# Performance work log

Measured on AMD Instinct MI355X. Metric: run time of the kernel, lower is better.

## Reference

```python
import jax, jax.numpy as jnp
import numpy as np

B, S, D, E, H, K = 4, 2048, 1024, 8, 1024, 2


def setup_inputs() -> dict:
    key = jax.random.key(0)
    k0, k1, k2, k3 = jax.random.split(key, 4)
    x = jax.random.normal(k0, (B, S, D), dtype=jnp.float32)
    router_w = jax.random.normal(k1, (E, D), dtype=jnp.float32) * 0.02
    w1 = jax.random.normal(k2, (D, E * H), dtype=jnp.float32) * 0.02
    w2 = jax.random.normal(k3, (E * H, D), dtype=jnp.float32) * 0.02
    expert_bias = jnp.zeros((E,), dtype=jnp.float32)
    return {"x": x, "router_w": router_w, "w1": w1, "w2": w2, "expert_bias": expert_bias}


def reference(x, router_w, w1, w2, expert_bias):
    b, s, d = x.shape
    e = router_w.shape[0]
    x_flat = x.reshape(-1, d)                      # [T, D]
    T = x_flat.shape[0]

    # Router: sigmoid scores, bias-balanced top-k selection
    router_logits = x_flat @ router_w.T            # [T, E]
    router_probs = jax.nn.sigmoid(router_logits.astype(jnp.float32))
    selection_scores = router_probs + expert_bias[None, :]
    _, selected = jax.lax.top_k(selection_scores, K)          # [T, K] indices
    top_k_w = jnp.take_along_axis(router_probs, selected, axis=-1)
    top_k_w = top_k_w / (top_k_w.sum(-1, keepdims=True) + 1e-20)
    top_k_w = top_k_w.astype(x.dtype)

    # Combine weights as a sparse [T, E] matrix (equivalent to the
    # padded_gather / grouped-GEMM / padded_scatter pipeline since
    # unselected experts get weight 0).
    combine = jnp.zeros((T, e), dtype=x.dtype).at[
        jnp.arange(T)[:, None], selected].add(top_k_w)

    # Expert MLP: relu(x @ w1)^2 @ w2, experts are contiguous column blocks
    h = jnp.square(jax.nn.relu(x_flat @ w1))       # [T, E*H]
    h = h.reshape(T, e, H) * combine[:, :, None]   # weighted per-expert hidden
    y = jnp.einsum('teh,ehd->td', h, w2.reshape(e, H, d))
    output = y.reshape(b, s, d)

    # Aux losses
    router_z_loss = jnp.mean(jnp.square(jax.nn.logsumexp(router_logits, axis=-1)))
    sel_flat = selected.reshape(-1)
    tokens_per_expert = jnp.zeros((e,), jnp.float32).at[sel_flat].add(1.0)
    f_i = (tokens_per_expert / tokens_per_expert.sum()).astype(x.dtype)

    # bias-balancing branch: per-sequence load balance loss
    sel_seq = selected.reshape(b, s * K)
    f_seq = jnp.zeros((b, e), jnp.float32).at[
        jnp.arange(b)[:, None], sel_seq].add(1.0) / (s * K)
    p_seq = router_probs.reshape(b, s, e).mean(axis=1)
    load_balance_loss = e * (f_seq * p_seq).sum(-1).mean()

    # uniform expert widths -> normalized widths are all 1
    widths_norm = jnp.ones((e,), jnp.float32)
    compute_loss = (router_probs @ widths_norm).mean()

    return output, router_z_loss, load_balance_loss, compute_loss, f_i
```

## Files before the change

kernel.cpp:

```cpp
#include <hip/hip_runtime.h>

typedef unsigned short u16;
typedef unsigned int u32;
typedef __bf16 bf16x8 __attribute__((ext_vector_type(8)));
typedef float f32x4 __attribute__((ext_vector_type(4)));

#define NTOK   8192
#define DDIM   1024
#define NEXP   8
#define HDIM   1024
#define PAIRS  16384

__device__ __forceinline__ u16 f2bf(float f) {
  union { float f; u32 u; } v; v.f = f;
  u32 r = v.u + 0x7FFFu + ((v.u >> 16) & 1u);
  return (u16)(r >> 16);
}

__device__ __forceinline__ f32x4 mfma16(bf16x8 a, bf16x8 b, f32x4 c) {
  return __builtin_amdgcn_mfma_f32_16x16x32_bf16(a, b, c, 0, 0, 0);
}

__device__ __forceinline__ void gload16(const void* g, void* l) {
  __builtin_amdgcn_global_load_lds(
      (__attribute__((address_space(1))) void*)g,
      (__attribute__((address_space(3))) void*)l, 16, 0, 0);
}

__global__ __launch_bounds__(256) void transpose_all(
    const float* __restrict__ w1, const float* __restrict__ w2,
    u16* __restrict__ w1t, u16* __restrict__ w2t) {
  __shared__ float tile[32][33];
  int z = blockIdx.z;
  const float* ib; long rs; u16* ob;
  if (z < 8) { ib = w1 + z * 1024; rs = 8192; ob = w1t + (long)z * 1048576; }
  else       { ib = w2 + (long)(z - 8) * 1048576; rs = 1024; ob = w2t + (long)(z - 8) * 1048576; }
  int r0 = blockIdx.y * 32, c0 = blockIdx.x * 32;
  int tx = threadIdx.x & 31, ty = threadIdx.x >> 5;
  #pragma unroll
  for (int rr = 0; rr < 32; rr += 8)
    tile[ty + rr][tx] = ib[(long)(r0 + ty + rr) * rs + c0 + tx];
  __syncthreads();
  #pragma unroll
  for (int rr = 0; rr < 32; rr += 8)
    ob[(long)(c0 + ty + rr) * 1024 + r0 + tx] = f2bf(tile[tx][ty + rr]);
}

__global__ __launch_bounds__(256) void router_kernel(
    const float* __restrict__ x, const float* __restrict__ rw,
    const float* __restrict__ ebias, u16* __restrict__ xb,
    int2* __restrict__ sel, float2* __restrict__ selw,
    u32* __restrict__ cnt, u32* __restrict__ cnt_be,
    float* __restrict__ pe_sum, float* __restrict__ z_sum) {
  __shared__ float rw_lds[8 * 1028];
  __shared__ float pe_loc[8];
  __shared__ float z_loc;
  __shared__ u32 cl[8];
  int tid = threadIdx.x;
  for (int i = tid; i < 8192; i += 256)
    rw_lds[(i >> 10) * 1028 + (i & 1023)] = rw[i];
  if (tid < 8) { pe_loc[tid] = 0.f; cl[tid] = 0u; }
  if (tid == 8) z_loc = 0.f;
  __syncthreads();

  int ht = tid >> 5;
  int hl = tid & 31;
  int t = blockIdx.x * 8 + ht;
  const float* xr = x + (long)t * DDIM;
  u16* xbr = xb + (long)t * DDIM;
  double acc[8];
  #pragma unroll
  for (int e = 0; e < 8; e++) acc[e] = 0.0;
  #pragma unroll
  for (int p = 0; p < 8; p++) {
    int d = p * 128 + hl * 4;
    float4 xv = *(const float4*)(xr + d);
    *(ushort4*)(xbr + d) = make_ushort4(f2bf(xv.x), f2bf(xv.y), f2bf(xv.z), f2bf(xv.w));
    #pragma unroll
    for (int e = 0; e < 8; e++) {
      float4 wv = *(const float4*)(rw_lds + e * 1028 + d);
      acc[e] += (double)xv.x * (double)wv.x + (double)xv.y * (double)wv.y
              + (double)xv.z * (double)wv.z + (double)xv.w * (double)wv.w;
    }
  }
  #pragma unroll
  for (int e = 0; e < 8; e++) {
    #pragma unroll
    for (int off = 16; off > 0; off >>= 1)
      acc[e] += __shfl_down(acc[e], off, 32);
  }
  if (hl == 0) {
    double logit[8]; float p8[8], score[8];
    for (int e = 0; e < 8; e++) {
      logit[e] = acc[e];
      p8[e] = (float)(1.0 / (1.0 + exp(-logit[e])));
      score[e] = p8[e] + ebias[e];
    }
    int i0 = 0;
    for (int e = 1; e < 8; e++) if (score[e] > score[i0]) i0 = e;
    int i1 = (i0 == 0) ? 1 : 0;
    for (int e = 0; e < 8; e++) if (e != i0 && score[e] > score[i1]) i1 = e;
    float w0 = p8[i0], w1v = p8[i1];
    float ssum = w0 + w1v + 1e-20f;
    sel[t] = make_int2(i0, i1);
    selw[t] = make_float2(w0 / ssum, w1v / ssum);
    double m = logit[0];
    for (int e = 1; e < 8; e++) m = fmax(m, logit[e]);
    double se = 0.0;
    for (int e = 0; e < 8; e++) se += exp(logit[e] - m);
    double ls = m + log(se);
    atomicAdd(&z_loc, (float)(ls * ls));
    for (int e = 0; e < 8; e++) atomicAdd(&pe_loc[e], p8[e]);
    atomicAdd(&cl[i0], 1u); atomicAdd(&cl[i1], 1u);
  }
  __syncthreads();
  if (tid < 8) {
    int b = (int)((blockIdx.x * 8) >> 11);
    atomicAdd(&cnt[tid], cl[tid]);
    atomicAdd(&cnt_be[b * 8 + tid], cl[tid]);
    atomicAdd(&pe_sum[b * 8 + tid], pe_loc[tid]);
  }
  if (tid == 8) atomicAdd(z_sum, z_loc);
}

__global__ void offsets_kernel(const u32* __restrict__ cnt, u32* __restrict__ offs,
                               u32* __restrict__ cursor) {
  if (threadIdx.x == 0 && blockIdx.x == 0) {
    u32 a = 0;
    for (int e = 0; e < 8; e++) { offs[e] = a; cursor[e] = a; a += cnt[e]; }
  }
}

__global__ __launch_bounds__(256) void build_lists(
    const int2* __restrict__ sel, const float2* __restrict__ selw,
    u32* __restrict__ cursor, int* __restrict__ tok_list, float* __restrict__ wt_list,
    int* __restrict__ inv) {
  int t = blockIdx.x * 256 + threadIdx.x;
  int2 s = sel[t]; float2 w = selw[t];
  u32 p0 = atomicAdd(&cursor[s.x], 1u);
  tok_list[p0] = t; wt_list[p0] = w.x; inv[2 * t] = (int)p0;
  u32 p1 = atomicAdd(&cursor[s.y], 1u);
  tok_list[p1] = t; wt_list[p1] = w.y; inv[2 * t + 1] = (int)p1;
}

template <bool SECOND>
__global__ __launch_bounds__(256, 2) void moe_gemm(
    const u16* __restrict__ A, const u16* __restrict__ Bt,
    u16* __restrict__ out16,
    const int* __restrict__ tok_list, const float* __restrict__ wt_list,
    const u32* __restrict__ cnt, const u32* __restrict__ offs) {
  int tn = blockIdx.x & 7;
  int tm = blockIdx.x >> 3;
  int e = 0, acct = 0;
  while (e < 8) {
    int nt = (int)((cnt[e] + 127u) >> 7);
    if (tm < acct + nt) break;
    acct += nt; e++;
  }
  if (e == 8) return;
  int m0 = (tm - acct) * 128;
  int off = (int)offs[e];
  int ce  = (int)cnt[e];

  __shared__ uint4 smem[4096];

  int tid = threadIdx.x;
  int l = tid & 63, w = tid >> 6;

  const u16* agp[4]; const u16* bgp[4];
  #pragma unroll
  for (int j = 0; j < 4; j++) {
    int p = w * 256 + j * 64 + l;
    int row = p >> 3, c = p & 7;
    long arow;
    if (SECOND) {
      arow = (long)(off + m0 + row);
    } else {
      int rr = m0 + row; if (rr > ce - 1) rr = ce - 1;
      arow = (long)tok_list[off + rr];
    }
    agp[j] = A + arow * 1024 + c * 8;
    bgp[j] = Bt + (long)e * 1048576 + (long)(tn * 128 + row) * 1024 + c * 8;
  }

  #pragma unroll
  for (int j = 0; j < 4; j++) {
    gload16(agp[j], &smem[w * 256 + j * 64]);
    gload16(bgp[j], &smem[2048 + w * 256 + j * 64]);
    agp[j] += 64; bgp[j] += 64;
  }
  __syncthreads();

  f32x4 acc[4][4];
  #pragma unroll
  for (int i = 0; i < 4; i++)
    #pragma unroll
    for (int j = 0; j < 4; j++) acc[i][j] = (f32x4){0.f, 0.f, 0.f, 0.f};

  int mr = l & 15, q = l >> 4;
  int wm = (w >> 1) * 64, wn = (w & 1) * 64;

  for (int k = 0; k < 16; k++) {
    int cur = k & 1, nxt = cur ^ 1;
    if (k < 15) {
      #pragma unroll
      for (int j = 0; j < 4; j++) {
        gload16(agp[j], &smem[nxt * 1024 + w * 256 + j * 64]);
        gload16(bgp[j], &smem[2048 + nxt * 1024 + w * 256 + j * 64]);
        agp[j] += 64; bgp[j] += 64;
      }
    }
    const uint4* Ab = smem + cur * 1024;
    const uint4* Bb = smem + 2048 + cur * 1024;
    #pragma unroll
    for (int kk = 0; kk < 2; kk++) {
      int cg = kk * 4 + q;
      bf16x8 af[4], bfr[4];
      #pragma unroll
      for (int i = 0; i < 4; i++) {
        af[i]  = __builtin_bit_cast(bf16x8, Ab[(wm + i * 16 + mr) * 8 + cg]);
        bfr[i] = __builtin_bit_cast(bf16x8, Bb[(wn + i * 16 + mr) * 8 + cg]);
      }
      #pragma unroll
      for (int i = 0; i < 4; i++)
        #pragma unroll
        for (int j = 0; j < 4; j++)
          acc[i][j] = mfma16(af[i], bfr[j], acc[i][j]);
    }
    __syncthreads();
  }

  u16* ost = (u16*)smem + w * 4608;
  #pragma unroll
  for (int i = 0; i < 4; i++) {
    #pragma unroll
    for (int r = 0; r < 4; r++) {
      int rl = i * 16 + q * 4 + r;
      float wgt = 1.f;
      if (SECOND) {
        int gr = m0 + wm + rl;
        int slot = (gr < ce) ? (off + gr) : 0;
        wgt = wt_list[slot];
      }
      #pragma unroll
      for (int j = 0; j < 4; j++) {
        float v = acc[i][j][r];
        if (!SECOND) { v = fmaxf(v, 0.f); v = v * v; }
        else v *= wgt;
        ost[rl * 72 + j * 16 + mr] = f2bf(v);
      }
    }
  }
  #pragma unroll
  for (int pr = 0; pr < 8; pr++) {
    int rl = pr * 8 + (l >> 3);
    int c8 = l & 7;
    uint4 v = *(const uint4*)(ost + rl * 72 + c8 * 8);
    int gr = m0 + wm + rl;
    if (gr < ce)
      *(uint4*)(out16 + (long)(off + gr) * 1024 + tn * 128 + wn + c8 * 8) = v;
  }
}

__global__ __launch_bounds__(128) void combine_kernel(
    const u16* __restrict__ y, const int* __restrict__ inv,
    float* __restrict__ out) {
  int t = blockIdx.x, tid = threadIdx.x;
  int s0 = inv[2 * t], s1 = inv[2 * t + 1];
  uint4 a = *(const uint4*)(y + (long)s0 * 1024 + tid * 8);
  uint4 b = *(const uint4*)(y + (long)s1 * 1024 + tid * 8);
  float o[8];
  const u32* au = (const u32*)&a;
  const u32* bu = (const u32*)&b;
  #pragma unroll
  for (int i = 0; i < 4; i++) {
    union { u32 u; float f; } lo1, hi1, lo2, hi2;
    lo1.u = au[i] << 16;  hi1.u = au[i] & 0xFFFF0000u;
    lo2.u = bu[i] << 16;  hi2.u = bu[i] & 0xFFFF0000u;
    o[2 * i]     = lo1.f + lo2.f;
    o[2 * i + 1] = hi1.f + hi2.f;
  }
  float* op = out + (long)t * 1024 + tid * 8;
  *(float4*)op       = make_float4(o[0], o[1], o[2], o[3]);
  *(float4*)(op + 4) = make_float4(o[4], o[5], o[6], o[7]);
}

__global__ void finalize_kernel(
    const float* __restrict__ pe_sum, const float* __restrict__ z_sum,
    const u32* __restrict__ cnt, const u32* __restrict__ cnt_be,
    float* __restrict__ out_tail) {
  if (threadIdx.x == 0 && blockIdx.x == 0) {
    float z = z_sum[0] / (float)NTOK;
    float lb = 0.f, clv = 0.f;
    for (int p = 0; p < 32; p++) {
      float psum = pe_sum[p];
      clv += psum;
      float f = (float)cnt_be[p] / 4096.0f;
      lb += f * (psum / 2048.0f);
    }
    lb = 8.0f * lb / 4.0f;
    clv = clv / (float)NTOK;
    out_tail[0] = z;
    out_tail[1] = lb;
    out_tail[2] = clv;
    for (int e2 = 0; e2 < 8; e2++) out_tail[3 + e2] = (float)cnt[e2] / 16384.0f;
  }
}

extern "C" void kernel_launch(void* const* d_in, const int* in_sizes, int n_in,
                              void* d_out, int out_size, void* d_ws, size_t ws_size,
                              hipStream_t stream) {
  const float* x     = (const float*)d_in[0];
  const float* rw    = (const float*)d_in[1];
  const float* w1    = (const float*)d_in[2];
  const float* w2    = (const float*)d_in[3];
  const float* ebias = (const float*)d_in[4];
  float* out = (float*)d_out;

  char* ws = (char*)d_ws;
  u16*    xb        = (u16*)(ws + 0);
  u16*    w1t       = (u16*)(ws + 16777216);
  u16*    y         = (u16*)(ws + 0);
  u16*    w2t       = (u16*)(ws + 33554432);
  u16*    h         = (u16*)(ws + 50331648);
  int*    tok_list  = (int*)(ws + 84148224);
  float*  wt_list   = (float*)(ws + 84213760);
  int2*   sel       = (int2*)(ws + 84279296);
  float2* selw      = (float2*)(ws + 84344832);
  int*    inv       = (int*)(ws + 84705280);
  u32*    cnt       = (u32*)(ws + 84770816);
  u32*    cursor    = cnt + 8;
  u32*    cnt_be    = cnt + 16;
  u32*    offs      = cnt + 48;
  float*  pe_sum    = (float*)(cnt + 56);
  float*  z_sum     = (float*)(cnt + 88);

  hipMemsetAsync(cnt, 0, 512, stream);

  transpose_all<<<dim3(32, 32, 16), 256, 0, stream>>>(w1, w2, w1t, w2t);
  router_kernel<<<1024, 256, 0, stream>>>(x, rw, ebias, xb, sel, selw, cnt, cnt_be, pe_sum, z_sum);
  offsets_kernel<<<1, 64, 0, stream>>>(cnt, offs, cursor);
  build_lists<<<32, 256, 0, stream>>>(sel, selw, cursor, tok_list, wt_list, inv);
  moe_gemm<false><<<136 * 8, 256, 0, stream>>>(xb, w1t, h, tok_list, wt_list, cnt, offs);
  moe_gemm<true><<<136 * 8, 256, 0, stream>>>(h, w2t, y, tok_list, wt_list, cnt, offs);
  combine_kernel<<<8192, 128, 0, stream>>>(y, inv, out);
  finalize_kernel<<<1, 64, 0, stream>>>(pe_sum, z_sum, cnt, cnt_be, out + 8388608);
}
```

Measured before the change: 376.6 us.

## Merge prep kernels, fold finalize, remap GEMM tile order, widen combine blocks

Fuses the weight transpose, router, and offset computation into one launch, using a last-block ticket to write the expert offsets. Finalize is merged into build_lists, and combine now handles two tokens per 256-thread block. The GEMM block index is remapped so consecutive blocks span different M tiles, which changes the L2 locality and the XCD distribution. The aim is fewer kernel launches and less serialization between small kernels, at the cost of a heavier combined prep kernel whose transpose and router blocks contend for the device at the same time.

```diff
diff --git a/kernel.cpp b/kernel.cpp
--- a/kernel.cpp
+++ b/kernel.cpp
@@ -27,120 +27,149 @@
       (__attribute__((address_space(3))) void*)l, 16, 0, 0);
 }
 
-__global__ __launch_bounds__(256) void transpose_all(
+__global__ __launch_bounds__(256) void prep_kernel(
+    const float* __restrict__ x, const float* __restrict__ rw,
+    const float* __restrict__ ebias,
     const float* __restrict__ w1, const float* __restrict__ w2,
-    u16* __restrict__ w1t, u16* __restrict__ w2t) {
-  __shared__ float tile[32][33];
-  int z = blockIdx.z;
-  const float* ib; long rs; u16* ob;
-  if (z < 8) { ib = w1 + z * 1024; rs = 8192; ob = w1t + (long)z * 1048576; }
-  else       { ib = w2 + (long)(z - 8) * 1048576; rs = 1024; ob = w2t + (long)(z - 8) * 1048576; }
-  int r0 = blockIdx.y * 32, c0 = blockIdx.x * 32;
-  int tx = threadIdx.x & 31, ty = threadIdx.x >> 5;
-  #pragma unroll
-  for (int rr = 0; rr < 32; rr += 8)
-    tile[ty + rr][tx] = ib[(long)(r0 + ty + rr) * rs + c0 + tx];
-  __syncthreads();
-  #pragma unroll
-  for (int rr = 0; rr < 32; rr += 8)
-    ob[(long)(c0 + ty + rr) * 1024 + r0 + tx] = f2bf(tile[tx][ty + rr]);
-}
-
-__global__ __launch_bounds__(256) void router_kernel(
-    const float* __restrict__ x, const float* __restrict__ rw,
-    const float* __restrict__ ebias, u16* __restrict__ xb,
+    u16* __restrict__ xb, u16* __restrict__ w1t, u16* __restrict__ w2t,
     int2* __restrict__ sel, float2* __restrict__ selw,
     u32* __restrict__ cnt, u32* __restrict__ cnt_be,
-    float* __restrict__ pe_sum, float* __restrict__ z_sum) {
-  __shared__ float rw_lds[8 * 1028];
+    float* __restrict__ pe_sum, float* __restrict__ z_sum,
+    u32* __restrict__ offs, u32* __restrict__ cursor, u32* __restrict__ ticket) {
+  __shared__ float smem[8 * 1028];
   __shared__ float pe_loc[8];
   __shared__ float z_loc;
   __shared__ u32 cl[8];
   int tid = threadIdx.x;
-  for (int i = tid; i < 8192; i += 256)
-    rw_lds[(i >> 10) * 1028 + (i & 1023)] = rw[i];
-  if (tid < 8) { pe_loc[tid] = 0.f; cl[tid] = 0u; }
-  if (tid == 8) z_loc = 0.f;
+
+  if (blockIdx.x < 1024) {
+    for (int i = tid; i < 8192; i += 256)
+      smem[(i >> 10) * 1028 + (i & 1023)] = rw[i];
+    if (tid < 8) { pe_loc[tid] = 0.f; cl[tid] = 0u; }
+    if (tid == 8) z_loc = 0.f;
+    __syncthreads();
+
+    int ht = tid >> 5;
+    int hl = tid & 31;
+    int t = blockIdx.x * 8 + ht;
+    const float* xr = x + (long)t * DDIM;
+    u16* xbr = xb + (long)t * DDIM;
+    double acc[8];
+    #pragma unroll
+    for (int e = 0; e < 8; e++) acc[e] = 0.0;
+    #pragma unroll
+    for (int p = 0; p < 8; p++) {
+      int d = p * 128 + hl * 4;
+      float4 xv = *(const float4*)(xr + d);
+      *(ushort4*)(xbr + d) = make_ushort4(f2bf(xv.x), f2bf(xv.y), f2bf(xv.z), f2bf(xv.w));
+      #pragma unroll
+      for (int e = 0; e < 8; e++) {
+        float4 wv = *(const float4*)(smem + e * 1028 + d);
+        acc[e] += (double)xv.x * (double)wv.x + (double)xv.y * (double)wv.y
+                + (double)xv.z * (double)wv.z + (double)xv.w * (double)wv.w;
+      }
+    }
+    #pragma unroll
+    for (int e = 0; e < 8; e++) {
+      #pragma unroll
+      for (int off = 16; off > 0; off >>= 1)
+        acc[e] += __shfl_down(acc[e], off, 32);
+    }
+    if (hl == 0) {
+      double logit[8]; float p8[8], score[8];
+      for (int e = 0; e < 8; e++) {
+        logit[e] = acc[e];
+        p8[e] = (float)(1.0 / (1.0 + exp(-logit[e])));
+        score[e] = p8[e] + ebias[e];
+      }
+      int i0 = 0;
+      for (int e = 1; e < 8; e++) if (score[e] > score[i0]) i0 = e;
+      int i1 = (i0 == 0) ? 1 : 0;
+      for (int e = 0; e < 8; e++) if (e != i0 && score[e] > score[i1]) i1 = e;
+      float w0 = p8[i0], w1v = p8[i1];
+      float ssum = w0 + w1v + 1e-20f;
+      sel[t] = make_int2(i0, i1);
+      selw[t] = make_float2(w0 / ssum, w1v / ssum);
+      double m = logit[0];
+      for (int e = 1; e < 8; e++) m = fmax(m, logit[e]);
+      double se = 0.0;
+      for (int e = 0; e < 8; e++) se += exp(logit[e] - m);
+      double ls = m + log(se);
+      atomicAdd(&z_loc, (float)(ls * ls));
+      for (int e = 0; e < 8; e++) atomicAdd(&pe_loc[e], p8[e]);
+      atomicAdd(&cl[i0], 1u); atomicAdd(&cl[i1], 1u);
+    }
+    __syncthreads();
+    if (tid < 8) {
+      int b = (int)((blockIdx.x * 8) >> 11);
+      atomicAdd(&cnt[tid], cl[tid]);
+      atomicAdd(&cnt_be[b * 8 + tid], cl[tid]);
+      atomicAdd(&pe_sum[b * 8 + tid], pe_loc[tid]);
+    }
+    if (tid == 8) atomicAdd(z_sum, z_loc);
+  } else {
+    float (*tile)[33] = (float(*)[33])smem;
+    int bid = blockIdx.x - 1024;
+    int z = bid >> 10;
+    int by = (bid >> 5) & 31, bx = bid & 31;
+    const float* ib; long rs; u16* ob;
+    if (z < 8) { ib = w1 + z * 1024; rs = 8192; ob = w1t + (long)z * 1048576; }
+    else       { ib = w2 + (long)(z - 8) * 1048576; rs = 1024; ob = w2t + (long)(z - 8) * 1048576; }
+    int r0 = by * 32, c0 = bx * 32;
+    int tx = tid & 31, ty = tid >> 5;
+    #pragma unroll
+    for (int rr = 0; rr < 32; rr += 8)
+      tile[ty + rr][tx] = ib[(long)(r0 + ty + rr) * rs + c0 + tx];
+    __syncthreads();
+    #pragma unroll
+    for (int rr = 0; rr < 32; rr += 8)
+      ob[(long)(c0 + ty + rr) * 1024 + r0 + tx] = f2bf(tile[tx][ty + rr]);
+  }
+
   __syncthreads();
-
-  int ht = tid >> 5;
-  int hl = tid & 31;
-  int t = blockIdx.x * 8 + ht;
-  const float* xr = x + (long)t * DDIM;
-  u16* xbr = xb + (long)t * DDIM;
-  double acc[8];
-  #pragma unroll
-  for (int e = 0; e < 8; e++) acc[e] = 0.0;
-  #pragma unroll
-  for (int p = 0; p < 8; p++) {
-    int d = p * 128 + hl * 4;
-    float4 xv = *(const float4*)(xr + d);
-    *(ushort4*)(xbr + d) = make_ushort4(f2bf(xv.x), f2bf(xv.y), f2bf(xv.z), f2bf(xv.w));
-    #pragma unroll
-    for (int e = 0; e < 8; e++) {
-      float4 wv = *(const float4*)(rw_lds + e * 1028 + d);
-      acc[e] += (double)xv.x * (double)wv.x + (double)xv.y * (double)wv.y
-              + (double)xv.z * (double)wv.z + (double)xv.w * (double)wv.w;
-    }
-  }
-  #pragma unroll
-  for (int e = 0; e < 8; e++) {
-    #pragma unroll
-    for (int off = 16; off > 0; off >>= 1)
-      acc[e] += __shfl_down(acc[e], off, 32);
-  }
-  if (hl == 0) {
-    double logit[8]; float p8[8], score[8];
-    for (int e = 0; e < 8; e++) {
-      logit[e] = acc[e];
-      p8[e] = (float)(1.0 / (1.0 + exp(-logit[e])));
-      score[e] = p8[e] + ebias[e];
-    }
-    int i0 = 0;
-    for (int e = 1; e < 8; e++) if (score[e] > score[i0]) i0 = e;
-    int i1 = (i0 == 0) ? 1 : 0;
-    for (int e = 0; e < 8; e++) if (e != i0 && score[e] > score[i1]) i1 = e;
-    float w0 = p8[i0], w1v = p8[i1];
-    float ssum = w0 + w1v + 1e-20f;
-    sel[t] = make_int2(i0, i1);
-    selw[t] = make_float2(w0 / ssum, w1v / ssum);
-    double m = logit[0];
-    for (int e = 1; e < 8; e++) m = fmax(m, logit[e]);
-    double se = 0.0;
-    for (int e = 0; e < 8; e++) se += exp(logit[e] - m);
-    double ls = m + log(se);
-    atomicAdd(&z_loc, (float)(ls * ls));
-    for (int e = 0; e < 8; e++) atomicAdd(&pe_loc[e], p8[e]);
-    atomicAdd(&cl[i0], 1u); atomicAdd(&cl[i1], 1u);
-  }
-  __syncthreads();
-  if (tid < 8) {
-    int b = (int)((blockIdx.x * 8) >> 11);
-    atomicAdd(&cnt[tid], cl[tid]);
-    atomicAdd(&cnt_be[b * 8 + tid], cl[tid]);
-    atomicAdd(&pe_sum[b * 8 + tid], pe_loc[tid]);
-  }
-  if (tid == 8) atomicAdd(z_sum, z_loc);
-}
-
-__global__ void offsets_kernel(const u32* __restrict__ cnt, u32* __restrict__ offs,
-                               u32* __restrict__ cursor) {
-  if (threadIdx.x == 0 && blockIdx.x == 0) {
-    u32 a = 0;
-    for (int e = 0; e < 8; e++) { offs[e] = a; cursor[e] = a; a += cnt[e]; }
-  }
-}
-
-__global__ __launch_bounds__(256) void build_lists(
+  if (tid == 0) {
+    __threadfence();
+    u32 tk = atomicAdd(ticket, 1u);
+    if (tk == gridDim.x - 1) {
+      u32 a = 0;
+      for (int e = 0; e < 8; e++) {
+        u32 c = atomicAdd(&cnt[e], 0u);
+        offs[e] = a; cursor[e] = a; a += c;
+      }
+    }
+  }
+}
+
+__global__ __launch_bounds__(256) void build_finalize(
     const int2* __restrict__ sel, const float2* __restrict__ selw,
     u32* __restrict__ cursor, int* __restrict__ tok_list, float* __restrict__ wt_list,
-    int* __restrict__ inv) {
+    int* __restrict__ inv,
+    const float* __restrict__ pe_sum, const float* __restrict__ z_sum,
+    const u32* __restrict__ cnt, const u32* __restrict__ cnt_be,
+    float* __restrict__ out_tail) {
   int t = blockIdx.x * 256 + threadIdx.x;
   int2 s = sel[t]; float2 w = selw[t];
   u32 p0 = atomicAdd(&cursor[s.x], 1u);
   tok_list[p0] = t; wt_list[p0] = w.x; inv[2 * t] = (int)p0;
   u32 p1 = atomicAdd(&cursor[s.y], 1u);
   tok_list[p1] = t; wt_list[p1] = w.y; inv[2 * t + 1] = (int)p1;
+
+  if (blockIdx.x == 0 && threadIdx.x == 0) {
+    float z = z_sum[0] / (float)NTOK;
+    float lb = 0.f, clv = 0.f;
+    for (int p = 0; p < 32; p++) {
+      float psum = pe_sum[p];
+      clv += psum;
+      float f = (float)cnt_be[p] / 4096.0f;
+      lb += f * (psum / 2048.0f);
+    }
+    lb = 8.0f * lb / 4.0f;
+    clv = clv / (float)NTOK;
+    out_tail[0] = z;
+    out_tail[1] = lb;
+    out_tail[2] = clv;
+    for (int e2 = 0; e2 < 8; e2++) out_tail[3 + e2] = (float)cnt[e2] / 16384.0f;
+  }
 }
 
 template <bool SECOND>
@@ -149,8 +178,10 @@
     u16* __restrict__ out16,
     const int* __restrict__ tok_list, const float* __restrict__ wt_list,
     const u32* __restrict__ cnt, const u32* __restrict__ offs) {
-  int tn = blockIdx.x & 7;
-  int tm = blockIdx.x >> 3;
+  int q8 = blockIdx.x & 7;
+  int r  = blockIdx.x >> 3;
+  int tn = r & 7;
+  int tm = q8 * 17 + (r >> 3);
   int e = 0, acct = 0;
   while (e < 8) {
     int nt = (int)((cnt[e] + 127u) >> 7);
@@ -234,8 +265,8 @@
   #pragma unroll
   for (int i = 0; i < 4; i++) {
     #pragma unroll
-    for (int r = 0; r < 4; r++) {
-      int rl = i * 16 + q * 4 + r;
+    for (int rr = 0; rr < 4; rr++) {
+      int rl = i * 16 + q * 4 + rr;
       float wgt = 1.f;
       if (SECOND) {
         int gr = m0 + wm + rl;
@@ -244,7 +275,7 @@
       }
       #pragma unroll
       for (int j = 0; j < 4; j++) {
-        float v = acc[i][j][r];
+        float v = acc[i][j][rr];
         if (!SECOND) { v = fmaxf(v, 0.f); v = v * v; }
         else v *= wgt;
         ost[rl * 72 + j * 16 + mr] = f2bf(v);
@@ -262,10 +293,11 @@
   }
 }
 
-__global__ __launch_bounds__(128) void combine_kernel(
+__global__ __launch_bounds__(256) void combine_kernel(
     const u16* __restrict__ y, const int* __restrict__ inv,
     float* __restrict__ out) {
-  int t = blockIdx.x, tid = threadIdx.x;
+  int t = blockIdx.x * 2 + (threadIdx.x >> 7);
+  int tid = threadIdx.x & 127;
   int s0 = inv[2 * t], s1 = inv[2 * t + 1];
   uint4 a = *(const uint4*)(y + (long)s0 * 1024 + tid * 8);
   uint4 b = *(const uint4*)(y + (long)s1 * 1024 + tid * 8);
@@ -283,28 +315,6 @@
   float* op = out + (long)t * 1024 + tid * 8;
   *(float4*)op       = make_float4(o[0], o[1], o[2], o[3]);
   *(float4*)(op + 4) = make_float4(o[4], o[5], o[6], o[7]);
-}
-
-__global__ void finalize_kernel(
-    const float* __restrict__ pe_sum, const float* __restrict__ z_sum,
-    const u32* __restrict__ cnt, const u32* __restrict__ cnt_be,
-    float* __restrict__ out_tail) {
-  if (threadIdx.x == 0 && blockIdx.x == 0) {
-    float z = z_sum[0] / (float)NTOK;
-    float lb = 0.f, clv = 0.f;
-    for (int p = 0; p < 32; p++) {
-      float psum = pe_sum[p];
-      clv += psum;
-      float f = (float)cnt_be[p] / 4096.0f;
-      lb += f * (psum / 2048.0f);
-    }
-    lb = 8.0f * lb / 4.0f;
-    clv = clv / (float)NTOK;
-    out_tail[0] = z;
-    out_tail[1] = lb;
-    out_tail[2] = clv;
-    for (int e2 = 0; e2 < 8; e2++) out_tail[3 + e2] = (float)cnt[e2] / 16384.0f;
-  }
 }
 
 extern "C" void kernel_launch(void* const* d_in, const int* in_sizes, int n_in,
@@ -334,15 +344,16 @@
   u32*    offs      = cnt + 48;
   float*  pe_sum    = (float*)(cnt + 56);
   float*  z_sum     = (float*)(cnt + 88);
+  u32*    ticket    = cnt + 96;
 
   hipMemsetAsync(cnt, 0, 512, stream);
 
-  transpose_all<<<dim3(32, 32, 16), 256, 0, stream>>>(w1, w2, w1t, w2t);
-  router_kernel<<<1024, 256, 0, stream>>>(x, rw, ebias, xb, sel, selw, cnt, cnt_be, pe_sum, z_sum);
-  offsets_kernel<<<1, 64, 0, stream>>>(cnt, offs, cursor);
-  build_lists<<<32, 256, 0, stream>>>(sel, selw, cursor, tok_list, wt_list, inv);
+  prep_kernel<<<1024 + 16384, 256, 0, stream>>>(
+      x, rw, ebias, w1, w2, xb, w1t, w2t, sel, selw,
+      cnt, cnt_be, pe_sum, z_sum, offs, cursor, ticket);
+  build_finalize<<<32, 256, 0, stream>>>(sel, selw, cursor, tok_list, wt_list, inv,
+                                         pe_sum, z_sum, cnt, cnt_be, out + 8388608);
   moe_gemm<false><<<136 * 8, 256, 0, stream>>>(xb, w1t, h, tok_list, wt_list, cnt, offs);
   moe_gemm<true><<<136 * 8, 256, 0, stream>>>(h, w2t, y, tok_list, wt_list, cnt, offs);
-  combine_kernel<<<8192, 128, 0, stream>>>(y, inv, out);
-  finalize_kernel<<<1, 64, 0, stream>>>(pe_sum, z_sum, cnt, cnt_be, out + 8388608);
-}
+  combine_kernel<<<4096, 256, 0, stream>>>(y, inv, out);
+}
```

Result: slower. 1.014 ms (+169.3%).
